# Optimization experiments

Measured on AMD Instinct MI355X. Metric: run time of the kernel, lower is better.

The kernel has to match this reference:

```python
import jax, jax.numpy as jnp
import numpy as np

B, N, L = 1, 2048, 256
DX, DY, H = 1536, 768, 12
D = DX // H  # head_dim = 128
EPS_MOD = 1e-6   # modulated_rmsnorm eps
EPS_QK = 1e-5    # per-head RMSNorm eps


def setup_inputs() -> dict:
    key = jax.random.key(0)
    ks = jax.random.split(key, 16)
    def n(k, shape, s=1.0):
        return jax.random.normal(k, shape, dtype=jnp.float32) * s
    # rotary tables: (N, H, D//2), shared across heads
    pos = jnp.arange(N, dtype=jnp.float32)
    inv_freq = 1.0 / (10000.0 ** (jnp.arange(D // 2, dtype=jnp.float32) / (D // 2)))
    ang = pos[:, None] * inv_freq[None, :]                       # (N, D/2)
    rope_cos = jnp.broadcast_to(jnp.cos(ang)[:, None, :], (N, H, D // 2))
    rope_sin = jnp.broadcast_to(jnp.sin(ang)[:, None, :], (N, H, D // 2))
    return {
        "x": n(ks[0], (B, N, DX)),
        "y": n(ks[1], (B, L, DY)),
        "scale_x": n(ks[2], (B, DX), 0.1),
        "scale_y": n(ks[3], (B, DY), 0.1),
        "rope_cos": rope_cos,
        "rope_sin": rope_sin,
        "Wqkv_x": n(ks[4], (DX, 3 * DX), 0.02),
        "bqkv_x": jnp.zeros((3 * DX,), jnp.float32),
        "Wqkv_y": n(ks[5], (DY, 3 * DX), 0.02),
        "bqkv_y": jnp.zeros((3 * DX,), jnp.float32),
        "q_norm_x_w": jnp.ones((D,), jnp.float32),
        "k_norm_x_w": jnp.ones((D,), jnp.float32),
        "q_norm_y_w": jnp.ones((D,), jnp.float32),
        "k_norm_y_w": jnp.ones((D,), jnp.float32),
        "Wproj_x": n(ks[6], (DX, DX), 0.02),
        "bproj_x": jnp.zeros((DX,), jnp.float32),
        "Wproj_y": n(ks[7], (DX, DY), 0.02),
        "bproj_y": jnp.zeros((DY,), jnp.float32),
    }


def _rms(v, eps):
    return v * jax.lax.rsqrt(jnp.mean(v * v, axis=-1, keepdims=True) + eps)


def _rope(q, cos, sin):
    # q: (B, S, H, D); cos/sin: (S, H, D/2); even/odd interleaved rotation
    qe, qo = q[..., 0::2], q[..., 1::2]
    re = qe * cos - qo * sin
    ro = qe * sin + qo * cos
    return jnp.stack([re, ro], axis=-1).reshape(q.shape)


def reference(x, y, scale_x, scale_y, rope_cos, rope_sin,
              Wqkv_x, bqkv_x, Wqkv_y, bqkv_y,
              q_norm_x_w, k_norm_x_w, q_norm_y_w, k_norm_y_w,
              Wproj_x, bproj_x, Wproj_y, bproj_y):
    b, n, dx = x.shape
    _, l, _ = y.shape
    h, d = H, D
    # --- visual stream ---
    xm = _rms(x, EPS_MOD) * (1.0 + scale_x[:, None, :])          # modulated_rmsnorm
    qkv = (xm @ Wqkv_x + bqkv_x).reshape(b, n, 3, h, d)
    q_x, k_x, v_x = qkv[:, :, 0], qkv[:, :, 1], qkv[:, :, 2]
    q_x = _rope(_rms(q_x, EPS_QK) * q_norm_x_w, rope_cos, rope_sin)
    k_x = _rope(_rms(k_x, EPS_QK) * k_norm_x_w, rope_cos, rope_sin)
    # --- text stream ---
    ym = _rms(y, EPS_MOD) * (1.0 + scale_y[:, None, :])
    qkvy = (ym @ Wqkv_y + bqkv_y).reshape(b, l, 3, h, d)
    q_y, k_y, v_y = qkvy[:, :, 0], qkvy[:, :, 1], qkvy[:, :, 2]
    q_y = _rms(q_y, EPS_QK) * q_norm_y_w
    k_y = _rms(k_y, EPS_QK) * k_norm_y_w
    # --- joint attention over concatenated sequence (B, H, N+L, D) ---
    q = jnp.concatenate([q_x, q_y], axis=1).transpose(0, 2, 1, 3)
    k = jnp.concatenate([k_x, k_y], axis=1).transpose(0, 2, 1, 3)
    v = jnp.concatenate([v_x, v_y], axis=1).transpose(0, 2, 1, 3)
    scale = 1.0 / np.sqrt(d).astype(np.float32)
    attn = jax.nn.softmax(jnp.einsum('bhqd,bhkd->bhqk', q, k) * scale, axis=-1)
    out = jnp.einsum('bhqk,bhkd->bhqd', attn, v)
    out = out.transpose(0, 2, 1, 3).reshape(b, n + l, h * d)
    x_out = out[:, :n] @ Wproj_x + bproj_x
    y_out = out[:, n:] @ Wproj_y + bproj_y
    return (x_out, y_out)
```

## Files before the change

kernel.cpp:

```cpp
#include <hip/hip_runtime.h>

typedef unsigned short u16;
typedef __attribute__((ext_vector_type(8))) short short8;
typedef __attribute__((ext_vector_type(4))) short short4v;
typedef __attribute__((ext_vector_type(4))) float floatx4;

__device__ __forceinline__ u16 f2bf(float f) {
  return (u16)((__float_as_uint(f) + 0x8000u) >> 16);
}
__device__ __forceinline__ float bf2f(u16 v) {
  return __uint_as_float(((unsigned)v) << 16);
}
__device__ __forceinline__ unsigned cvt_pk_bf16(float a, float b) {
  unsigned r;
  asm("v_cvt_pk_bf16_f32 %0, %1, %2" : "=v"(r) : "v"(a), "v"(b));
  return r;
}

#define GLD16(g, l) __builtin_amdgcn_global_load_lds( \
    (const __attribute__((address_space(1))) void*)(g), \
    (__attribute__((address_space(3))) void*)(l), 16, 0, 0)

__global__ __launch_bounds__(256) void prep(const float* __restrict__ W0, u16* __restrict__ T0,
                                            const float* __restrict__ W1, u16* __restrict__ T1,
                                            const float* __restrict__ W2, u16* __restrict__ T2,
                                            const float* __restrict__ W3, u16* __restrict__ T3,
                                            const float* __restrict__ x, const float* __restrict__ scale_x,
                                            const float* __restrict__ y, const float* __restrict__ scale_y,
                                            u16* __restrict__ xm, u16* __restrict__ ym) {
  __shared__ float t[32][33];
  const int z = blockIdx.z;
  if (z < 4) {
    const float* in; u16* out; int K, N;
    switch (z) {
      case 0: in = W0; out = T0; K = 1536; N = 4608; break;
      case 1: in = W1; out = T1; K = 768;  N = 4608; break;
      case 2: in = W2; out = T2; K = 1536; N = 1536; break;
      default: in = W3; out = T3; K = 1536; N = 768; break;
    }
    const int n0 = blockIdx.x * 32, k0 = blockIdx.y * 32;
    if (n0 >= N || k0 >= K) return;
    const int tx = threadIdx.x, ty = threadIdx.y;
#pragma unroll
    for (int i = 0; i < 32; i += 8)
      t[ty + i][tx] = in[(size_t)(k0 + ty + i) * N + n0 + tx];
    __syncthreads();
#pragma unroll
    for (int i = 0; i < 32; i += 8)
      out[(size_t)(n0 + ty + i) * K + k0 + tx] = f2bf(t[tx][ty + i]);
  } else {
    const int row = blockIdx.y * 144 + blockIdx.x;
    if (row >= 2304) return;
    const int tid = threadIdx.y * 32 + threadIdx.x;
    const float* xr; const float* sc; u16* dst; int D;
    if (row < 2048) { D = 1536; xr = x + (size_t)row * D; sc = scale_x; dst = xm + (size_t)row * D; }
    else { D = 768; xr = y + (size_t)(row - 2048) * D; sc = scale_y; dst = ym + (size_t)(row - 2048) * D; }
    float ss = 0.f;
    for (int c = tid; c < D; c += 256) { float v = xr[c]; ss += v * v; }
    for (int off = 32; off > 0; off >>= 1) ss += __shfl_down(ss, off);
    __shared__ float red[4];
    if ((tid & 63) == 0) red[tid >> 6] = ss;
    __syncthreads();
    const float tot = red[0] + red[1] + red[2] + red[3];
    const float r = rsqrtf(tot / (float)D + 1e-6f);
    for (int c = tid; c < D; c += 256)
      dst[c] = f2bf(xr[c] * r * (1.0f + sc[c]));
  }
}

template <bool BOUT>
__global__ __launch_bounds__(256) void gemm2(const u16* __restrict__ A0, const u16* __restrict__ BT0,
                                             const float* __restrict__ bias0, void* __restrict__ C0,
                                             int M0, int N0, int K0,
                                             const u16* __restrict__ A1, const u16* __restrict__ BT1,
                                             const float* __restrict__ bias1, void* __restrict__ C1,
                                             int M1, int N1, int K1) {
  const u16 *A, *BT; const float* bias; void* Cout; int M, N, K;
  if (blockIdx.z == 0) { A = A0; BT = BT0; bias = bias0; Cout = C0; M = M0; N = N0; K = K0; }
  else { A = A1; BT = BT1; bias = bias1; Cout = C1; M = M1; N = N1; K = K1; }
  const int nty = M >> 7, ntx = N >> 7;
  const int W = ntx * nty;
  const int bid = blockIdx.x;
  const int xcd = bid & 7, local = bid >> 3;
  const int q = W >> 3, r = W & 7;
  const int cap = (xcd < r) ? q + 1 : q;
  if (local >= cap) return;
  const int w = (xcd < r) ? xcd * (q + 1) + local
                          : r * (q + 1) + (xcd - r) * q + local;
  const int tx = w / nty, ty = w - tx * nty;
  const int bm = ty * 128, bn = tx * 128;

  __shared__ __align__(16) u16 As[3][128 * 32];
  __shared__ __align__(16) u16 Bs[3][128 * 32];
  const int tid = threadIdx.x;
  const int lane = tid & 63, wave = tid >> 6;
  const int wm = (wave & 1) * 64, wn = (wave >> 1) * 64;
  const int row16 = lane & 15, quad = lane >> 4;

  floatx4 acc[4][4] = {};
  const int r0 = lane >> 2, c4 = (lane & 3) * 8;
  const u16* Ag0 = A + (size_t)(bm + wave * 16 + r0) * K + c4;
  const u16* Ag1 = A + (size_t)(bm + (wave + 4) * 16 + r0) * K + c4;
  const u16* Bg0 = BT + (size_t)(bn + wave * 16 + r0) * K + c4;
  const u16* Bg1 = BT + (size_t)(bn + (wave + 4) * 16 + r0) * K + c4;
  const int d0 = wave * 512, d1 = (wave + 4) * 512;

  GLD16(Ag0, &As[0][d0]);
  GLD16(Ag1, &As[0][d1]);
  GLD16(Bg0, &Bs[0][d0]);
  GLD16(Bg1, &Bs[0][d1]);
  GLD16(Ag0 + 32, &As[1][d0]);
  GLD16(Ag1 + 32, &As[1][d1]);
  GLD16(Bg0 + 32, &Bs[1][d0]);
  GLD16(Bg1 + 32, &Bs[1][d1]);

  int cur = 0;
  for (int k0 = 0; k0 < K; k0 += 32) {
    if (k0 + 64 < K) {
      int nxt2 = cur + 2; if (nxt2 >= 3) nxt2 -= 3;
      GLD16(Ag0 + k0 + 64, &As[nxt2][d0]);
      GLD16(Ag1 + k0 + 64, &As[nxt2][d1]);
      GLD16(Bg0 + k0 + 64, &Bs[nxt2][d0]);
      GLD16(Bg1 + k0 + 64, &Bs[nxt2][d1]);
      asm volatile("s_waitcnt vmcnt(8)" ::: "memory");
    } else if (k0 + 32 < K) {
      asm volatile("s_waitcnt vmcnt(4)" ::: "memory");
    } else {
      asm volatile("s_waitcnt vmcnt(0)" ::: "memory");
    }
    __builtin_amdgcn_s_barrier();
    asm volatile("" ::: "memory");
    short8 af[4], bf[4];
#pragma unroll
    for (int i = 0; i < 4; i++) {
      af[i] = *(const short8*)&As[cur][(wm + i * 16 + row16) * 32 + quad * 8];
      bf[i] = *(const short8*)&Bs[cur][(wn + i * 16 + row16) * 32 + quad * 8];
    }
#pragma unroll
    for (int mi = 0; mi < 4; mi++)
#pragma unroll
      for (int ni = 0; ni < 4; ni++)
        acc[mi][ni] = __builtin_amdgcn_mfma_f32_16x16x32_bf16(af[mi], bf[ni], acc[mi][ni], 0, 0, 0);
    asm volatile("" ::: "memory");
    __builtin_amdgcn_s_barrier();
    cur += 1; if (cur >= 3) cur -= 3;
  }
#pragma unroll
  for (int mi = 0; mi < 4; mi++) {
#pragma unroll
    for (int ni = 0; ni < 4; ni++) {
      const int col = bn + wn + ni * 16 + row16;
      const float b = bias[col];
      const int row0 = bm + wm + mi * 16 + quad * 4;
#pragma unroll
      for (int r2 = 0; r2 < 4; r2++) {
        const float v = acc[mi][ni][r2] + b;
        if constexpr (BOUT)
          ((u16*)Cout)[(size_t)(row0 + r2) * N + col] = f2bf(v);
        else
          ((float*)Cout)[(size_t)(row0 + r2) * N + col] = v;
      }
    }
  }
}

__global__ __launch_bounds__(256) void qkv_post(const u16* __restrict__ qkvx,
                                                const u16* __restrict__ qkvy,
                                                const float* __restrict__ qnwx, const float* __restrict__ knwx,
                                                const float* __restrict__ qnwy, const float* __restrict__ knwy,
                                                const float* __restrict__ rcos, const float* __restrict__ rsin,
                                                u16* __restrict__ Q, u16* __restrict__ Kb, u16* __restrict__ Vt) {
  const int s0 = blockIdx.x * 32, h = blockIdx.y;
  const int tid = threadIdx.x, wave = tid >> 6, lane = tid & 63;
  const int sl = wave * 8 + (lane >> 3);
  const int s = s0 + sl;
  const int d0 = (lane & 7) * 16;
  const bool isx = s < 2048;
  const u16* base = isx ? (qkvx + (size_t)s * 4608) : (qkvy + (size_t)(s - 2048) * 4608);

  const short8 qv0 = *(const short8*)(base + h * 128 + d0);
  const short8 qv1 = *(const short8*)(base + h * 128 + d0 + 8);
  const short8 kv0 = *(const short8*)(base + 1536 + h * 128 + d0);
  const short8 kv1 = *(const short8*)(base + 1536 + h * 128 + d0 + 8);
  const short8 vv0 = *(const short8*)(base + 3072 + h * 128 + d0);
  const short8 vv1 = *(const short8*)(base + 3072 + h * 128 + d0 + 8);

  float q[16], k[16];
#pragma unroll
  for (int j = 0; j < 8; j++) {
    q[j] = bf2f((u16)qv0[j]); q[j + 8] = bf2f((u16)qv1[j]);
    k[j] = bf2f((u16)kv0[j]); k[j + 8] = bf2f((u16)kv1[j]);
  }
  float sq = 0.f, sk = 0.f;
#pragma unroll
  for (int j = 0; j < 16; j++) { sq += q[j] * q[j]; sk += k[j] * k[j]; }
#pragma unroll
  for (int off = 1; off <= 4; off <<= 1) { sq += __shfl_xor(sq, off); sk += __shfl_xor(sk, off); }
  const float rq = rsqrtf(sq * (1.f / 128.f) + 1e-5f);
  const float rk = rsqrtf(sk * (1.f / 128.f) + 1e-5f);

  const float* qw = isx ? qnwx : qnwy;
  const float* kw = isx ? knwx : knwy;
#pragma unroll
  for (int j = 0; j < 16; j++) {
    q[j] = q[j] * rq * qw[d0 + j];
    k[j] = k[j] * rk * kw[d0 + j];
  }
  if (isx) {
    const float* cb = rcos + ((size_t)s * 12 + h) * 64 + (d0 >> 1);
    const float* sb = rsin + ((size_t)s * 12 + h) * 64 + (d0 >> 1);
#pragma unroll
    for (int p = 0; p < 8; p++) {
      const float c = cb[p], sn = sb[p];
      const float qe = q[2 * p], qo = q[2 * p + 1];
      const float ke = k[2 * p], ko = k[2 * p + 1];
      q[2 * p] = qe * c - qo * sn; q[2 * p + 1] = qe * sn + qo * c;
      k[2 * p] = ke * c - ko * sn; k[2 * p + 1] = ke * sn + ko * c;
    }
  }
  u16 qo16[16], ko16[16];
#pragma unroll
  for (int j = 0; j < 16; j++) {
    qo16[j] = f2bf(q[j] * 0.12751737942f);
    ko16[j] = f2bf(k[j]);
  }
  const size_t o = ((size_t)h * 2304 + s) * 128 + d0;
  *(short8*)(Q + o) = *(const short8*)&qo16[0];
  *(short8*)(Q + o + 8) = *(const short8*)&qo16[8];
  *(short8*)(Kb + o) = *(const short8*)&ko16[0];
  *(short8*)(Kb + o + 8) = *(const short8*)&ko16[8];

  __shared__ u16 vlds[128][33];
#pragma unroll
  for (int j = 0; j < 8; j++) {
    vlds[d0 + j][sl] = (u16)vv0[j];
    vlds[d0 + 8 + j][sl] = (u16)vv1[j];
  }
  __syncthreads();
  const int row = tid >> 1, sc = (tid & 1) * 16;
  u16 tmp[16];
#pragma unroll
  for (int j = 0; j < 16; j++) tmp[j] = vlds[row][sc + j];
  u16* vdst = Vt + ((size_t)h * 128 + row) * 2304 + s0 + sc;
  *(short8*)vdst = *(const short8*)&tmp[0];
  *(short8*)(vdst + 8) = *(const short8*)&tmp[8];
}

__global__ __launch_bounds__(256, 3) void attn(const u16* __restrict__ Q, const u16* __restrict__ Kb,
                                               const u16* __restrict__ Vt,
                                               u16* __restrict__ Opart,
                                               float* __restrict__ Mp, float* __restrict__ Lp) {
  const int bid = blockIdx.x;
  const int xcd = bid & 7, local = bid >> 3;
  const int slot = local / 18, qt = local % 18;
  const int combo = slot * 8 + xcd;
  if (combo >= 36) return;
  const int h = combo % 12, split = combo / 12;
  const int q0 = qt * 128;
  const int tid = threadIdx.x, lane = tid & 63, wave = tid >> 6;
  const int row16 = lane & 15, quad = lane >> 4;
  const u16* Qh = Q + (size_t)h * 2304 * 128;
  const u16* Kh = Kb + (size_t)h * 2304 * 128;
  const u16* Vh = Vt + (size_t)h * 128 * 2304;

  __shared__ __align__(16) u16 Ks[64 * 128];
  __shared__ __align__(16) u16 Vs[128 * 64];
  __shared__ __align__(16) u16 Ps[4][32 * 64];

  short8 qf[2][4];
#pragma unroll
  for (int g = 0; g < 2; g++) {
    const u16* qrow = Qh + (size_t)(q0 + wave * 32 + g * 16 + row16) * 128;
#pragma unroll
    for (int kk = 0; kk < 4; kk++) qf[g][kk] = *(const short8*)(qrow + kk * 32 + quad * 8);
  }
  floatx4 oacc[2][8] = {};
  float m_i[2] = {-1e30f, -1e30f}, l_i[2] = {0.f, 0.f};

  const u16* Kp[4]; const u16* Vp[4];
#pragma unroll
  for (int i = 0; i < 4; i++) {
    const int j = i * 4 + wave;
    const int krow = j * 4 + (lane >> 4);
    const int kcol = ((lane & 15) ^ (krow & 7)) * 8;
    const int vrow = j * 8 + (lane >> 3);
    const int vcol = ((lane & 7) ^ (vrow & 7)) * 8;
    Kp[i] = Kh + (size_t)krow * 128 + kcol;
    Vp[i] = Vh + (size_t)vrow * 2304 + vcol;
  }
  const int sw = row16 & 7;
  const int kbeg = split * 768, kend = kbeg + 768;

  for (int kt = kbeg; kt < kend; kt += 64) {
    __syncthreads();
#pragma unroll
    for (int i = 0; i < 4; i++) {
      GLD16(Kp[i] + (size_t)kt * 128, Ks + (i * 4 + wave) * 512);
      GLD16(Vp[i] + kt, Vs + (i * 4 + wave) * 512);
    }
    __syncthreads();

    floatx4 sacc[2][4] = {};
#pragma unroll
    for (int mk = 0; mk < 4; mk++) {
#pragma unroll
      for (int kk = 0; kk < 4; kk++) {
        const int c = (4 * kk + quad) ^ sw;
        const short8 kfrag = *(const short8*)&Ks[(mk * 16 + row16) * 128 + c * 8];
        sacc[0][mk] = __builtin_amdgcn_mfma_f32_16x16x32_bf16(kfrag, qf[0][kk], sacc[0][mk], 0, 0, 0);
        sacc[1][mk] = __builtin_amdgcn_mfma_f32_16x16x32_bf16(kfrag, qf[1][kk], sacc[1][mk], 0, 0, 0);
      }
    }
#pragma unroll
    for (int g = 0; g < 2; g++) {
      float mx = sacc[g][0][0];
#pragma unroll
      for (int mk = 0; mk < 4; mk++)
#pragma unroll
        for (int r = 0; r < 4; r++) mx = fmaxf(mx, sacc[g][mk][r]);
      mx = fmaxf(mx, __shfl_xor(mx, 16));
      mx = fmaxf(mx, __shfl_xor(mx, 32));
      if (__any(mx > m_i[g] + 8.f)) {
        const float mnew = fmaxf(m_i[g], mx);
        const float alpha = __builtin_amdgcn_exp2f(m_i[g] - mnew);
        m_i[g] = mnew;
        const float a0 = __shfl(alpha, quad * 4 + 0);
        const float a1 = __shfl(alpha, quad * 4 + 1);
        const float a2 = __shfl(alpha, quad * 4 + 2);
        const float a3 = __shfl(alpha, quad * 4 + 3);
#pragma unroll
        for (int nd = 0; nd < 8; nd++) {
          oacc[g][nd][0] *= a0; oacc[g][nd][1] *= a1; oacc[g][nd][2] *= a2; oacc[g][nd][3] *= a3;
        }
        l_i[g] *= alpha;
      }
      float s = 0.f;
#pragma unroll
      for (int mk = 0; mk < 4; mk++)
#pragma unroll
        for (int r = 0; r < 4; r++) {
          const float p = __builtin_amdgcn_exp2f(sacc[g][mk][r] - m_i[g]);
          sacc[g][mk][r] = p;
          s += p;
        }
      s += __shfl_xor(s, 16);
      s += __shfl_xor(s, 32);
      l_i[g] += s;
    }

#pragma unroll
    for (int g = 0; g < 2; g++)
#pragma unroll
      for (int mk = 0; mk < 4; mk++) {
        const int subp = (4 * mk + quad) ^ (sw << 1);
        uint2 pk;
        pk.x = cvt_pk_bf16(sacc[g][mk][0], sacc[g][mk][1]);
        pk.y = cvt_pk_bf16(sacc[g][mk][2], sacc[g][mk][3]);
        *(uint2*)&Ps[wave][(g * 16 + row16) * 64 + subp * 4] = pk;
      }
    const int pc0 = quad ^ sw, pc1 = (4 + quad) ^ sw;
    short8 pf[2][2];
#pragma unroll
    for (int g = 0; g < 2; g++) {
      pf[g][0] = *(const short8*)&Ps[wave][(g * 16 + row16) * 64 + pc0 * 8];
      pf[g][1] = *(const short8*)&Ps[wave][(g * 16 + row16) * 64 + pc1 * 8];
    }
#pragma unroll
    for (int nd = 0; nd < 8; nd++) {
      const short8 vf0 = *(const short8*)&Vs[(nd * 16 + row16) * 64 + pc0 * 8];
      const short8 vf1 = *(const short8*)&Vs[(nd * 16 + row16) * 64 + pc1 * 8];
      oacc[0][nd] = __builtin_amdgcn_mfma_f32_16x16x32_bf16(pf[0][0], vf0, oacc[0][nd], 0, 0, 0);
      oacc[0][nd] = __builtin_amdgcn_mfma_f32_16x16x32_bf16(pf[0][1], vf1, oacc[0][nd], 0, 0, 0);
      oacc[1][nd] = __builtin_amdgcn_mfma_f32_16x16x32_bf16(pf[1][0], vf0, oacc[1][nd], 0, 0, 0);
      oacc[1][nd] = __builtin_amdgcn_mfma_f32_16x16x32_bf16(pf[1][1], vf1, oacc[1][nd], 0, 0, 0);
    }
  }
#pragma unroll
  for (int g = 0; g < 2; g++) {
    const size_t base = (size_t)(split * 12 + h) * 2304 + q0 + wave * 32 + g * 16;
#pragma unroll
    for (int nd = 0; nd < 8; nd++)
#pragma unroll
      for (int r = 0; r < 4; r++)
        Opart[(base + quad * 4 + r) * 128 + nd * 16 + row16] = f2bf(oacc[g][nd][r]);
    if (lane < 16) { Mp[base + lane] = m_i[g]; Lp[base + lane] = l_i[g]; }
  }
}

__global__ __launch_bounds__(256) void attn_combine(const u16* __restrict__ Opart,
                                                    const float* __restrict__ Mp,
                                                    const float* __restrict__ Lp,
                                                    u16* __restrict__ attnout) {
  const int idx = blockIdx.x * 256 + threadIdx.x;
  const int dd = (idx & 31) * 4;
  const int hq = idx >> 5;
  const int h = hq % 12, q = hq / 12;
  size_t b[3]; float ms[3], ls[3];
  float m = -1e30f;
#pragma unroll
  for (int s = 0; s < 3; s++) {
    b[s] = (size_t)(s * 12 + h) * 2304 + q;
    ms[s] = Mp[b[s]]; ls[s] = Lp[b[s]];
    m = fmaxf(m, ms[s]);
  }
  float w[3], denom = 0.f;
#pragma unroll
  for (int s = 0; s < 3; s++) { w[s] = exp2f(ms[s] - m); denom += ls[s] * w[s]; }
  const float inv = 1.0f / denom;
  float ox = 0.f, oy = 0.f, oz = 0.f, ow = 0.f;
#pragma unroll
  for (int s = 0; s < 3; s++) {
    const short4v o = *(const short4v*)&Opart[b[s] * 128 + dd];
    ox += bf2f((u16)o[0]) * w[s]; oy += bf2f((u16)o[1]) * w[s];
    oz += bf2f((u16)o[2]) * w[s]; ow += bf2f((u16)o[3]) * w[s];
  }
  short4v out;
  out[0] = (short)f2bf(ox * inv);
  out[1] = (short)f2bf(oy * inv);
  out[2] = (short)f2bf(oz * inv);
  out[3] = (short)f2bf(ow * inv);
  *(short4v*)&attnout[(size_t)idx * 4] = out;
}

extern "C" void kernel_launch(void* const* d_in, const int* in_sizes, int n_in,
                              void* d_out, int out_size, void* d_ws, size_t ws_size,
                              hipStream_t stream) {
  const float* x        = (const float*)d_in[0];
  const float* y        = (const float*)d_in[1];
  const float* scale_x  = (const float*)d_in[2];
  const float* scale_y  = (const float*)d_in[3];
  const float* rope_cos = (const float*)d_in[4];
  const float* rope_sin = (const float*)d_in[5];
  const float* Wqkv_x   = (const float*)d_in[6];
  const float* bqkv_x   = (const float*)d_in[7];
  const float* Wqkv_y   = (const float*)d_in[8];
  const float* bqkv_y   = (const float*)d_in[9];
  const float* qnwx     = (const float*)d_in[10];
  const float* knwx     = (const float*)d_in[11];
  const float* qnwy     = (const float*)d_in[12];
  const float* knwy     = (const float*)d_in[13];
  const float* Wproj_x  = (const float*)d_in[14];
  const float* bproj_x  = (const float*)d_in[15];
  const float* Wproj_y  = (const float*)d_in[16];
  const float* bproj_y  = (const float*)d_in[17];
  float* out = (float*)d_out;

  char* ws = (char*)d_ws;
  size_t off = 0;
  auto take = [&](size_t bytes) { char* p = ws + off; off += (bytes + 255) & ~(size_t)255; return p; };
  u16* WqkvxT  = (u16*)take((size_t)4608 * 1536 * 2);
  u16* WqkvyT  = (u16*)take((size_t)4608 * 768 * 2);
  u16* WprojxT = (u16*)take((size_t)1536 * 1536 * 2);
  u16* WprojyT = (u16*)take((size_t)768 * 1536 * 2);
  u16* xm      = (u16*)take((size_t)2048 * 1536 * 2);
  u16* ym      = (u16*)take((size_t)256 * 768 * 2);
  u16* qkvx    = (u16*)take((size_t)2048 * 4608 * 2);
  u16* qkvy    = (u16*)take((size_t)256 * 4608 * 2);
  u16* Qb      = (u16*)take((size_t)12 * 2304 * 128 * 2);
  u16* Kb      = (u16*)take((size_t)12 * 2304 * 128 * 2);
  u16* Vt      = (u16*)take((size_t)12 * 128 * 2304 * 2);
  u16* attnout = (u16*)take((size_t)2304 * 1536 * 2);
  u16* Opart   = (u16*)take((size_t)3 * 12 * 2304 * 128 * 2);
  float* Mp    = (float*)take((size_t)3 * 12 * 2304 * 4);
  float* Lp    = (float*)take((size_t)3 * 12 * 2304 * 4);

  prep<<<dim3(144, 48, 5), dim3(32, 8), 0, stream>>>(Wqkv_x, WqkvxT, Wqkv_y, WqkvyT,
                                                     Wproj_x, WprojxT, Wproj_y, WprojyT,
                                                     x, scale_x, y, scale_y, xm, ym);

  gemm2<true><<<dim3(576, 1, 2), 256, 0, stream>>>(xm, WqkvxT, bqkv_x, qkvx, 2048, 4608, 1536,
                                                   ym, WqkvyT, bqkv_y, qkvy, 256, 4608, 768);

  qkv_post<<<dim3(72, 12), 256, 0, stream>>>(qkvx, qkvy, qnwx, knwx, qnwy, knwy,
                                             rope_cos, rope_sin, Qb, Kb, Vt);

  attn<<<dim3(720), 256, 0, stream>>>(Qb, Kb, Vt, Opart, Mp, Lp);
  attn_combine<<<(2304 * 1536 / 4) / 256, 256, 0, stream>>>(Opart, Mp, Lp, attnout);

  gemm2<false><<<dim3(192, 1, 2), 256, 0, stream>>>(attnout, WprojxT, bproj_x, out, 2048, 1536, 1536,
                                                    attnout + (size_t)2048 * 1536, WprojyT, bproj_y,
                                                    out + (size_t)2048 * 1536, 256, 768, 1536);
  (void)in_sizes; (void)n_in; (void)out_size; (void)ws_size;
}
```

Before: 298.6 us.

## Split output projection GEMM into three K slices with separate merge kernel

```diff
diff --git a/kernel.cpp b/kernel.cpp
--- a/kernel.cpp
+++ b/kernel.cpp
@@ -162,6 +162,114 @@
       }
     }
   }
+}
+
+__global__ __launch_bounds__(256) void gemm_splitk(const u16* __restrict__ A0, const u16* __restrict__ BT0,
+                                                   float* __restrict__ C0, int M0, int N0, int K0,
+                                                   const u16* __restrict__ A1, const u16* __restrict__ BT1,
+                                                   float* __restrict__ C1, int M1, int N1, int K1) {
+  const u16 *A, *BT; float* Cp; int M, N, K;
+  if (blockIdx.z == 0) { A = A0; BT = BT0; Cp = C0; M = M0; N = N0; K = K0; }
+  else { A = A1; BT = BT1; Cp = C1; M = M1; N = N1; K = K1; }
+  const int nty = M >> 7, ntx = N >> 7;
+  const int W = ntx * nty;
+  const int split = blockIdx.x % 3, w = blockIdx.x / 3;
+  if (w >= W) return;
+  const int tx = w / nty, ty = w - tx * nty;
+  const int bm = ty * 128, bn = tx * 128;
+  const int Ks = K / 3;
+  Cp += (size_t)split * M * N;
+
+  __shared__ __align__(16) u16 As[3][128 * 32];
+  __shared__ __align__(16) u16 Bs[3][128 * 32];
+  const int tid = threadIdx.x;
+  const int lane = tid & 63, wave = tid >> 6;
+  const int wm = (wave & 1) * 64, wn = (wave >> 1) * 64;
+  const int row16 = lane & 15, quad = lane >> 4;
+
+  floatx4 acc[4][4] = {};
+  const int r0 = lane >> 2, c4 = (lane & 3) * 8 + split * Ks;
+  const u16* Ag0 = A + (size_t)(bm + wave * 16 + r0) * K + c4;
+  const u16* Ag1 = A + (size_t)(bm + (wave + 4) * 16 + r0) * K + c4;
+  const u16* Bg0 = BT + (size_t)(bn + wave * 16 + r0) * K + c4;
+  const u16* Bg1 = BT + (size_t)(bn + (wave + 4) * 16 + r0) * K + c4;
+  const int d0 = wave * 512, d1 = (wave + 4) * 512;
+
+  GLD16(Ag0, &As[0][d0]);
+  GLD16(Ag1, &As[0][d1]);
+  GLD16(Bg0, &Bs[0][d0]);
+  GLD16(Bg1, &Bs[0][d1]);
+  GLD16(Ag0 + 32, &As[1][d0]);
+  GLD16(Ag1 + 32, &As[1][d1]);
+  GLD16(Bg0 + 32, &Bs[1][d0]);
+  GLD16(Bg1 + 32, &Bs[1][d1]);
+
+  int cur = 0;
+  for (int k0 = 0; k0 < Ks; k0 += 32) {
+    if (k0 + 64 < Ks) {
+      int nxt2 = cur + 2; if (nxt2 >= 3) nxt2 -= 3;
+      GLD16(Ag0 + k0 + 64, &As[nxt2][d0]);
+      GLD16(Ag1 + k0 + 64, &As[nxt2][d1]);
+      GLD16(Bg0 + k0 + 64, &Bs[nxt2][d0]);
+      GLD16(Bg1 + k0 + 64, &Bs[nxt2][d1]);
+      asm volatile("s_waitcnt vmcnt(8)" ::: "memory");
+    } else if (k0 + 32 < Ks) {
+      asm volatile("s_waitcnt vmcnt(4)" ::: "memory");
+    } else {
+      asm volatile("s_waitcnt vmcnt(0)" ::: "memory");
+    }
+    __builtin_amdgcn_s_barrier();
+    asm volatile("" ::: "memory");
+    short8 af[4], bf[4];
+#pragma unroll
+    for (int i = 0; i < 4; i++) {
+      af[i] = *(const short8*)&As[cur][(wm + i * 16 + row16) * 32 + quad * 8];
+      bf[i] = *(const short8*)&Bs[cur][(wn + i * 16 + row16) * 32 + quad * 8];
+    }
+#pragma unroll
+    for (int mi = 0; mi < 4; mi++)
+#pragma unroll
+      for (int ni = 0; ni < 4; ni++)
+        acc[mi][ni] = __builtin_amdgcn_mfma_f32_16x16x32_bf16(af[mi], bf[ni], acc[mi][ni], 0, 0, 0);
+    asm volatile("" ::: "memory");
+    __builtin_amdgcn_s_barrier();
+    cur += 1; if (cur >= 3) cur -= 3;
+  }
+#pragma unroll
+  for (int mi = 0; mi < 4; mi++) {
+#pragma unroll
+    for (int ni = 0; ni < 4; ni++) {
+      const int col = bn + wn + ni * 16 + row16;
+      const int row0 = bm + wm + mi * 16 + quad * 4;
+#pragma unroll
+      for (int r2 = 0; r2 < 4; r2++)
+        Cp[(size_t)(row0 + r2) * N + col] = acc[mi][ni][r2];
+    }
+  }
+}
+
+__global__ __launch_bounds__(256) void proj_merge(const float* __restrict__ Px,
+                                                  const float* __restrict__ Py,
+                                                  const float* __restrict__ bx,
+                                                  const float* __restrict__ by,
+                                                  float* __restrict__ out) {
+  const int z = blockIdx.z;
+  const float* P; const float* bias; float* o; int N; size_t total;
+  if (z == 0) { P = Px; bias = bx; o = out; N = 1536; total = (size_t)2048 * 1536; }
+  else { P = Py; bias = by; o = out + (size_t)2048 * 1536; N = 768; total = (size_t)256 * 768; }
+  const size_t idx4 = ((size_t)blockIdx.x * 256 + threadIdx.x) * 4;
+  if (idx4 >= total) return;
+  const int col = (int)(idx4 % (size_t)N);
+  const float4 p0 = *(const float4*)&P[idx4];
+  const float4 p1 = *(const float4*)&P[total + idx4];
+  const float4 p2 = *(const float4*)&P[2 * total + idx4];
+  const float4 bv = *(const float4*)&bias[col];
+  float4 r;
+  r.x = p0.x + p1.x + p2.x + bv.x;
+  r.y = p0.y + p1.y + p2.y + bv.y;
+  r.z = p0.z + p1.z + p2.z + bv.z;
+  r.w = p0.w + p1.w + p2.w + bv.w;
+  *(float4*)&o[idx4] = r;
 }
 
 __global__ __launch_bounds__(256) void qkv_post(const u16* __restrict__ qkvx,
@@ -463,6 +571,8 @@
   u16* Opart   = (u16*)take((size_t)3 * 12 * 2304 * 128 * 2);
   float* Mp    = (float*)take((size_t)3 * 12 * 2304 * 4);
   float* Lp    = (float*)take((size_t)3 * 12 * 2304 * 4);
+  float* Cpx = (float*)xm;
+  float* Cpy = (float*)WqkvxT;
 
   prep<<<dim3(144, 48, 5), dim3(32, 8), 0, stream>>>(Wqkv_x, WqkvxT, Wqkv_y, WqkvyT,
                                                      Wproj_x, WprojxT, Wproj_y, WprojyT,
@@ -477,8 +587,9 @@
   attn<<<dim3(720), 256, 0, stream>>>(Qb, Kb, Vt, Opart, Mp, Lp);
   attn_combine<<<(2304 * 1536 / 4) / 256, 256, 0, stream>>>(Opart, Mp, Lp, attnout);
 
-  gemm2<false><<<dim3(192, 1, 2), 256, 0, stream>>>(attnout, WprojxT, bproj_x, out, 2048, 1536, 1536,
-                                                    attnout + (size_t)2048 * 1536, WprojyT, bproj_y,
-                                                    out + (size_t)2048 * 1536, 256, 768, 1536);
+  gemm_splitk<<<dim3(576, 1, 2), 256, 0, stream>>>(attnout, WprojxT, Cpx, 2048, 1536, 1536,
+                                                   attnout + (size_t)2048 * 1536, WprojyT, Cpy,
+                                                   256, 768, 1536);
+  proj_merge<<<dim3(3072, 1, 2), 256, 0, stream>>>(Cpx, Cpy, bproj_x, bproj_y, out);
   (void)in_sizes; (void)n_in; (void)out_size; (void)ws_size;
 }
```

New measurement: 294.5 us. No clear change (-1.4%).
